# Kernel optimization log

Measured on AMD Instinct MI355X. Metric: run time of the kernel, lower is better.

## Reference

```python
import jax, jax.numpy as jnp
import numpy as np

N_NODES = 100000
N_EDGES = 3200000
DIMS = [32, 256, 1024, 1024, 256, 6]


def setup_inputs() -> dict:
    key = jax.random.key(0)
    ks = jax.random.split(key, 2 + 2 * 5)
    inp = {
        "x": jax.random.normal(ks[0], (N_NODES, DIMS[0]), dtype=jnp.float32),
        "edge_index": jax.random.randint(ks[1], (2, N_EDGES), 0, N_NODES, dtype=jnp.int64),
    }
    for i in range(5):
        fan_in, fan_out = DIMS[i], DIMS[i + 1]
        scale = (2.0 / (fan_in + fan_out)) ** 0.5  # glorot-ish
        inp[f"W{i+1}"] = jax.random.normal(ks[2 + 2 * i], (fan_in, fan_out), dtype=jnp.float32) * scale
        inp[f"b{i+1}"] = jnp.zeros((fan_out,), dtype=jnp.float32)
    return inp


def _gcn_forward(x, edge_index, Ws, bs):
    N = x.shape[0]
    # add self loops (PyG GCNConv default)
    loop = jnp.arange(N, dtype=edge_index.dtype)
    src = jnp.concatenate([edge_index[0], loop])
    dst = jnp.concatenate([edge_index[1], loop])
    # symmetric normalization: deg computed on target index (gcn_norm)
    deg = jax.ops.segment_sum(jnp.ones_like(dst, dtype=x.dtype), dst, num_segments=N)
    dinv = jnp.where(deg > 0, jax.lax.rsqrt(deg), 0.0)
    norm = (dinv[src] * dinv[dst])[:, None]  # [E+N, 1]

    def conv(h, W, b):
        h = h @ W                                    # dense linear
        msg = h[src] * norm                          # gather + scale
        agg = jax.ops.segment_sum(msg, dst, num_segments=N)  # scatter-add
        return agg + b

    h = x
    for i in range(4):
        h = jax.nn.relu(conv(h, Ws[i], bs[i]))
    return conv(h, Ws[4], bs[4])


def reference(x, edge_index, W1, b1, W2, b2, W3, b3, W4, b4, W5, b5):
    return _gcn_forward(x, edge_index, (W1, W2, W3, W4, W5), (b1, b2, b3, b4, b5))
```

## Files before the change

kernel.cpp:

```cpp
#include <hip/hip_runtime.h>

typedef unsigned char u8;
typedef unsigned short u16;
typedef unsigned int u32;
typedef __bf16 bf16_t;
typedef bf16_t bf16x8 __attribute__((ext_vector_type(8)));
typedef float f32x4 __attribute__((ext_vector_type(4)));
typedef float f32x2 __attribute__((ext_vector_type(2)));

#define LDS_PTR(p) ((__attribute__((address_space(3))) unsigned int*)(p))
#define GLB_PTR(p) ((const __attribute__((address_space(1))) unsigned int*)(p))

#define BSH 9
#define BCAP 32768

static __device__ __forceinline__ float bf2f(u16 h) {
  u32 u = ((u32)h) << 16;
  return __builtin_bit_cast(float, u);
}
static __device__ __forceinline__ u16 f2bf(float f) {
  u32 u = __builtin_bit_cast(u32, f);
  u += 0x7fffu + ((u >> 16) & 1u);
  return (u16)(u >> 16);
}

static __device__ __forceinline__ int xcd_swizzle(int wg, int nwg) {
  const int q = nwg >> 3, r = nwg & 7;
  const int xcd = wg & 7, pos = wg >> 3;
  return (xcd < r ? xcd * (q + 1) : r * (q + 1) + (xcd - r) * q) + pos;
}

__global__ void detect_kernel(const int* __restrict__ ei, const u16* __restrict__ x,
                              int* __restrict__ flags, int* __restrict__ zp, int zn) {
  __shared__ int cnt;
  if (threadIdx.x == 0) cnt = 0;
  __syncthreads();
  if (blockIdx.x == 0) {
    if (ei[1 + 2 * threadIdx.x] != 0) atomicAdd(&cnt, 1);
    __syncthreads();
    if (threadIdx.x == 0) flags[0] = (cnt == 0) ? 1 : 0;
  } else if (blockIdx.x == 1) {
    u32 u = x[threadIdx.x];
    u32 e = (u >> 7) & 0xFF;
    if (e >= 0x60 && e <= 0x83) atomicAdd(&cnt, 1);
    __syncthreads();
    if (threadIdx.x == 0) flags[1] = (cnt >= 240) ? 0 : 1;
  } else {
    for (int i = threadIdx.x; i < zn; i += 256) zp[i] = 0;
  }
}

static __device__ __forceinline__ int eidx(const void* ei, size_t i, int m) {
  return m ? (int)((const long long*)ei)[i] : ((const int*)ei)[i];
}

__global__ void zero_out_kernel(void* __restrict__ out, int n, const int* __restrict__ flags) {
  int i = blockIdx.x * 256 + threadIdx.x;
  if (i < n) {
    if (flags[1]) ((float*)out)[i] = 0.0f;
    else ((u16*)out)[i] = 0;
  }
}

struct CvtArgs {
  const void* src[10];
  u16* dst[10];
  int K[10];
  int N[10];
  int start[11];
};
__global__ void convert_all_kernel(CvtArgs a, const int* __restrict__ flags) {
  int idx = blockIdx.x * 256 + threadIdx.x;
  int f32 = flags[1];
#pragma unroll
  for (int t = 0; t < 10; ++t) {
    if (idx >= a.start[t] && idx < a.start[t + 1]) {
      int local = idx - a.start[t];
      int K = a.K[t], N = a.N[t];
      int k = local / N, n = local - k * N;
      float v = f32 ? ((const float*)a.src[t])[local] : bf2f(((const u16*)a.src[t])[local]);
      a.dst[t][(size_t)n * K + k] = f2bf(v);
    }
  }
}

__global__ __launch_bounds__(256) void bin_kernel(const void* __restrict__ ei,
                                                  int* __restrict__ gcur,
                                                  int2* __restrict__ pairs, int E, int Nn,
                                                  const int* __restrict__ flags, int nblk) {
  __shared__ int h[256];
  __shared__ int base[256];
  const int m = flags[0];
  const int nb = (Nn + (1 << BSH) - 1) >> BSH;
  const int per = (E + nblk - 1) / nblk;
  const int e0 = blockIdx.x * per;
  const int e1 = (e0 + per < E) ? e0 + per : E;
  for (int i = threadIdx.x; i < nb; i += 256) h[i] = 0;
  __syncthreads();
  for (int e = e0 + threadIdx.x; e < e1; e += 256) {
    int d = eidx(ei, (size_t)E + e, m);
    if ((u32)d < (u32)Nn) atomicAdd(&h[d >> BSH], 1);
  }
  __syncthreads();
  for (int i = threadIdx.x; i < nb; i += 256) {
    base[i] = atomicAdd(&gcur[i], h[i]);
    h[i] = 0;
  }
  __syncthreads();
  for (int e = e0 + threadIdx.x; e < e1; e += 256) {
    int d = eidx(ei, (size_t)E + e, m);
    if ((u32)d >= (u32)Nn) continue;
    int s = eidx(ei, (size_t)e, m);
    if ((u32)s >= (u32)Nn) s = 0;
    int b = d >> BSH;
    int p = base[b] + atomicAdd(&h[b], 1);
    if (p < BCAP) pairs[(size_t)b * BCAP + p] = make_int2(s, d);
  }
}

__global__ __launch_bounds__(256) void bucket_scan_kernel(const int* __restrict__ gcur,
                                                          int* __restrict__ gbase, int NB) {
  __shared__ int sd[256];
  int tid = threadIdx.x;
  int v = (tid < NB) ? gcur[tid] : 0;
  if (v > BCAP) v = BCAP;
  sd[tid] = v;
  __syncthreads();
  for (int s = 1; s < 256; s <<= 1) {
    int t = (tid >= s) ? sd[tid - s] : 0;
    __syncthreads();
    sd[tid] += t;
    __syncthreads();
  }
  if (tid < NB) gbase[tid] = sd[tid] - v;
}

__global__ __launch_bounds__(512) void bucket_finalize_kernel(
    const int2* __restrict__ pairs, const int* __restrict__ gcur,
    const int* __restrict__ gbase, int* __restrict__ rowp, float* __restrict__ dinv,
    int* __restrict__ csr, int Nn) {
  __shared__ int cnt[512];
  __shared__ int scn[512];
  const int b = blockIdx.x;
  const int n0 = b << BSH;
  const int tid = threadIdx.x;
  cnt[tid] = 0;
  __syncthreads();
  int tot = gcur[b];
  if (tot > BCAP) tot = BCAP;
  for (int i = tid; i < tot; i += 512) {
    int2 pr = pairs[(size_t)b * BCAP + i];
    atomicAdd(&cnt[pr.y - n0], 1);
  }
  __syncthreads();
  int myc = cnt[tid];
  scn[tid] = myc;
  __syncthreads();
  for (int s = 1; s < 512; s <<= 1) {
    int t = (tid >= s) ? scn[tid - s] : 0;
    __syncthreads();
    scn[tid] += t;
    __syncthreads();
  }
  const int node = n0 + tid;
  const int start = gbase[b] + scn[tid] - myc;
  if (node < Nn) {
    rowp[node] = start;
    dinv[node] = rsqrtf((float)(myc + 1));
    if (node == Nn - 1) rowp[Nn] = gbase[b] + scn[tid];
  }
  cnt[tid] = start;
  __syncthreads();
  for (int i = tid; i < tot; i += 512) {
    int2 pr = pairs[(size_t)b * BCAP + i];
    int p = atomicAdd(&cnt[pr.y - n0], 1);
    csr[p] = pr.x;
  }
}

template <int NPW, int ACT, bool SRCF, bool DSTF, bool EDGEW>
__global__ __launch_bounds__(256) void spmm_narrow_kernel(
    const void* __restrict__ Hb, void* __restrict__ Gb,
    const int* __restrict__ rowp, const int* __restrict__ csr,
    const float* __restrict__ dinv, const u16* __restrict__ bias,
    int relu, int Nn, int src_stride, int dst_stride, const int* __restrict__ flags) {
  constexpr int G = 64 / NPW;
  constexpr int B = 16;
  const int lane = threadIdx.x & 63;
  const int col = lane & (G - 1);
  const int node = blockIdx.x * 4 * NPW + (threadIdx.x >> 6) * NPW + (lane / G);
  const bool anode = node < Nn;
  const bool act = anode && (col < ACT);
  int sf32 = 0, of32 = 0;
  if (SRCF) sf32 = flags[1];
  if (DSTF) of32 = flags[1];
  const u16* Hs = (const u16*)Hb;
  const float* Hf = (const float*)Hb;

  int e0 = 0, cnt = 0;
  if (anode) {
    e0 = rowp[node];
    cnt = rowp[node + 1] - e0;
  }
  float acc = 0.0f;
  for (int jb = 0; jb < cnt; jb += B) {
    int s[B];
#pragma unroll
    for (int j = 0; j < B; ++j) {
      bool val = (jb + j) < cnt;
      s[j] = val ? csr[e0 + jb + j] : node;
    }
    float wv[B];
    if constexpr (EDGEW) {
#pragma unroll
      for (int j = 0; j < B; ++j) wv[j] = ((jb + j) < cnt) ? dinv[s[j]] : 0.0f;
    }
    float v[B];
#pragma unroll
    for (int j = 0; j < B; ++j) {
      bool val = act && ((jb + j) < cnt);
      size_t idx = (size_t)s[j] * src_stride + col;
      v[j] = val ? ((SRCF && sf32) ? Hf[idx] : bf2f(Hs[idx])) : 0.0f;
    }
#pragma unroll
    for (int j = 0; j < B; ++j) {
      if constexpr (EDGEW) acc += wv[j] * v[j];
      else acc += v[j];
    }
  }
  if (!act) return;
  const float wi = dinv[node];
  {
    size_t idx = (size_t)node * src_stride + col;
    float sv = (SRCF && sf32) ? Hf[idx] : bf2f(Hs[idx]);
    if constexpr (EDGEW) acc += wi * sv;
    else acc += sv;
  }
  float v = acc * wi;
  if (bias) v += bf2f(bias[col]);
  if (relu) v = fmaxf(v, 0.0f);
  size_t didx = (size_t)node * dst_stride + col;
  if (DSTF && of32) ((float*)Gb)[didx] = v;
  else ((u16*)Gb)[didx] = f2bf(v);
}

template <int W>
__global__ __launch_bounds__(256) void spmm_fp8_kernel(
    const u8* __restrict__ Hq, u16* __restrict__ Gout,
    const int* __restrict__ rowp, const int* __restrict__ csr,
    const float* __restrict__ dinv, int n0, int n1, int dst_stride) {
  constexpr int BPL = W / 64;
  constexpr int ND = BPL / 4;
  constexpr int B = (W == 1024) ? 8 : 16;
  const int lane = threadIdx.x & 63;
  const int node = __builtin_amdgcn_readfirstlane(n0 + blockIdx.x * 4 + (threadIdx.x >> 6));
  if (node >= n1) return;
  const int off = lane * BPL;
  f32x2 acc[2 * ND] = {};

  auto dec1 = [&](const u32* d) {
#pragma unroll
    for (int q = 0; q < ND; ++q) {
      f32x2 a = __builtin_amdgcn_cvt_pk_f32_fp8((int)d[q], false);
      f32x2 b = __builtin_amdgcn_cvt_pk_f32_fp8((int)d[q], true);
      acc[2 * q] += a;
      acc[2 * q + 1] += b;
    }
  };
  auto ldrow = [&](u32* v, int s) {
    const u8* p = Hq + (size_t)s * W + off;
    if constexpr (ND == 4) *(int4*)v = *(const int4*)p;
    else v[0] = *(const u32*)p;
  };

  const int e0 = rowp[node];
  const int cnt = rowp[node + 1] - e0;
  const int tot = cnt + 1;
  const int NB2 = (tot + B - 1) / B;
  const int NBF = NB2 - 1;

  u32 vA[B][ND], vB[B][ND];

  auto ldb_full = [&](u32 (*v)[ND], int k) {
    const int base = k * B;
    int s[B];
#pragma unroll
    for (int j = 0; j < B; ++j) s[j] = csr[e0 + base + j];
#pragma unroll
    for (int j = 0; j < B; ++j) ldrow(v[j], s[j]);
  };
  auto ldb_last = [&](u32 (*v)[ND]) {
    const int base = NBF * B;
#pragma unroll
    for (int j = 0; j < B; ++j) {
      const int i = base + j;
      if (i < tot) {
        int s = (i < cnt) ? csr[e0 + i] : node;
        ldrow(v[j], s);
      } else {
#pragma unroll
        for (int q = 0; q < ND; ++q) v[j][q] = 0u;
      }
    }
  };
  auto decfull = [&](u32 (*v)[ND]) {
#pragma unroll
    for (int j = 0; j < B; ++j) dec1(v[j]);
  };

  if (NB2 == 1) {
    ldb_last(vA);
    decfull(vA);
  } else {
    ldb_last(vA);
    ldb_full(vB, 0);
    int k = 1;
    while (k + 1 < NBF) {
      decfull(vA);
      ldb_full(vA, k);
      decfull(vB);
      ldb_full(vB, k + 1);
      k += 2;
    }
    if (k < NBF) {
      decfull(vA);
      ldb_full(vA, k);
      decfull(vB);
      decfull(vA);
    } else {
      decfull(vA);
      decfull(vB);
    }
  }

  const float wi = dinv[node];
  u32 d[2 * ND];
#pragma unroll
  for (int kk = 0; kk < 2 * ND; ++kk) {
    float v0 = acc[kk].x * wi, v1 = acc[kk].y * wi;
    d[kk] = (u32)f2bf(v0) | ((u32)f2bf(v1) << 16);
  }
  u16* gp = Gout + (size_t)(node - n0) * dst_stride + off;
  if constexpr (ND == 4) {
    ((int4*)gp)[0] = make_int4((int)d[0], (int)d[1], (int)d[2], (int)d[3]);
    ((int4*)gp)[1] = make_int4((int)d[4], (int)d[5], (int)d[6], (int)d[7]);
  } else {
    *(int2*)gp = make_int2((int)d[0], (int)d[1]);
  }
}

__global__ __launch_bounds__(256) void spmm_u8_kernel(
    const u8* __restrict__ Hq, u16* __restrict__ G,
    const int* __restrict__ rowp, const int* __restrict__ csr,
    const float* __restrict__ dinv, const u32* __restrict__ maxbits,
    const u16* __restrict__ bias, int relu, int Nn, int dst_stride) {
  constexpr int B = 16;
  const int lane = threadIdx.x & 63;
  const int node = __builtin_amdgcn_readfirstlane(blockIdx.x * 4 + (threadIdx.x >> 6));
  if (node >= Nn) return;
  const int off = lane * 4;
  float mx = __builtin_bit_cast(float, *maxbits);
  float sq = mx > 0.0f ? mx * (1.0f / 127.0f) : 0.0f;
  float a0 = 0.0f, a1 = 0.0f, a2 = 0.0f, a3 = 0.0f, wsum = 0.0f;

  auto dec1 = [&](u32 d, float w) {
    a0 += w * (float)(d & 0xffu);
    a1 += w * (float)((d >> 8) & 0xffu);
    a2 += w * (float)((d >> 16) & 0xffu);
    a3 += w * (float)(d >> 24);
    wsum += w;
  };
  auto ldrow = [&](u32* v, int s) { *v = *(const u32*)(Hq + (size_t)s * 256 + off); };

  const int e0 = rowp[node];
  const int cnt = rowp[node + 1] - e0;
  const int tot = cnt + 1;
  const int NB2 = (tot + B - 1) / B;
  const int NBF = NB2 - 1;

  u32 vA[B], vB[B];
  float wA[B], wB[B];

  auto ldb_full = [&](u32* v, float* wv, int k) {
    const int base = k * B;
    int s[B];
#pragma unroll
    for (int j = 0; j < B; ++j) s[j] = csr[e0 + base + j];
#pragma unroll
    for (int j = 0; j < B; ++j) wv[j] = dinv[s[j]];
#pragma unroll
    for (int j = 0; j < B; ++j) ldrow(&v[j], s[j]);
  };
  auto ldb_last = [&](u32* v, float* wv) {
    const int base = NBF * B;
#pragma unroll
    for (int j = 0; j < B; ++j) {
      const int i = base + j;
      if (i < tot) {
        int s = (i < cnt) ? csr[e0 + i] : node;
        wv[j] = dinv[s];
        ldrow(&v[j], s);
      } else {
        v[j] = 0u;
        wv[j] = 0.0f;
      }
    }
  };
  auto decfull = [&](u32* v, float* wv) {
#pragma unroll
    for (int j = 0; j < B; ++j) dec1(v[j], wv[j]);
  };

  if (NB2 == 1) {
    ldb_last(vA, wA);
    decfull(vA, wA);
  } else {
    ldb_last(vA, wA);
    ldb_full(vB, wB, 0);
    int k = 1;
    while (k + 1 < NBF) {
      decfull(vA, wA);
      ldb_full(vA, wA, k);
      decfull(vB, wB);
      ldb_full(vB, wB, k + 1);
      k += 2;
    }
    if (k < NBF) {
      decfull(vA, wA);
      ldb_full(vA, wA, k);
      decfull(vB, wB);
      decfull(vA, wA);
    } else {
      decfull(vA, wA);
      decfull(vB, wB);
    }
  }

  const float wi = dinv[node];
  float su[4] = {a0, a1, a2, a3};
  float vals[4];
#pragma unroll
  for (int k2 = 0; k2 < 4; ++k2) {
    float v = (su[k2] - 128.0f * wsum) * wi * sq;
    if (bias) v += bf2f(bias[off + k2]);
    if (relu) v = fmaxf(v, 0.0f);
    vals[k2] = v;
  }
  u32 d0 = (u32)f2bf(vals[0]) | ((u32)f2bf(vals[1]) << 16);
  u32 d1 = (u32)f2bf(vals[2]) | ((u32)f2bf(vals[3]) << 16);
  *(int2*)(G + (size_t)node * dst_stride + off) = make_int2((int)d0, (int)d1);
}

__global__ void quant_kernel(const u16* __restrict__ t4, u8* __restrict__ t4q,
                             const u32* __restrict__ maxbits, int n4) {
  int i = blockIdx.x * 256 + threadIdx.x;
  if (i >= n4) return;
  float mx = __builtin_bit_cast(float, *maxbits);
  float inv = mx > 0.0f ? 127.0f / mx : 0.0f;
  int2 v = ((const int2*)t4)[i];
  float f0 = bf2f((u16)(v.x & 0xffff)), f1 = bf2f((u16)((u32)v.x >> 16));
  float f2 = bf2f((u16)(v.y & 0xffff)), f3 = bf2f((u16)((u32)v.y >> 16));
  int q0 = (int)rintf(f0 * inv), q1 = (int)rintf(f1 * inv);
  int q2 = (int)rintf(f2 * inv), q3 = (int)rintf(f3 * inv);
  q0 = min(127, max(-127, q0)) + 128; q1 = min(127, max(-127, q1)) + 128;
  q2 = min(127, max(-127, q2)) + 128; q3 = min(127, max(-127, q3)) + 128;
  ((u32*)t4q)[i] = (u32)q0 | ((u32)q1 << 8) | ((u32)q2 << 16) | ((u32)q3 << 24);
}

__global__ __launch_bounds__(256) void gemm_fast_kernel(
    const u16* __restrict__ A, int lda, const u16* __restrict__ Bt,
    u16* __restrict__ C, int ldc, const u16* __restrict__ bias,
    int M, int N, int K, int relu, int fp8out, u32* __restrict__ maxout,
    const float* __restrict__ rowscale) {
  __shared__ __align__(16) u16 sA[128 * 64];
  __shared__ __align__(16) u16 sB[128 * 64];
  const int tid = threadIdx.x;
  const int lane = tid & 63;
  const int wave = __builtin_amdgcn_readfirstlane(tid >> 6);
  const int gx = gridDim.x;
  int wg = blockIdx.y * gx + blockIdx.x;
  wg = xcd_swizzle(wg, gx * gridDim.y);
  const int m0 = (wg / gx) * 128, n0 = (wg % gx) * 128;
  const int wm = (wave & 1) * 64, wn = (wave >> 1) * 64;
  const int lr = lane & 15, lq = lane >> 4;
  const int lrow = lane >> 3;
  const int lcol = (lane & 7) * 8;
  f32x4 acc[4][4] = {};

  for (int kb = 0; kb < K; kb += 64) {
#pragma unroll
    for (int it = 0; it < 4; ++it) {
      const int rbase = (it * 4 + wave) * 8;
      int gm = m0 + rbase + lrow;
      if (gm >= M) gm = M - 1;
      __builtin_amdgcn_global_load_lds(GLB_PTR(A + (size_t)gm * lda + kb + lcol),
                                       LDS_PTR(sA + rbase * 64), 16, 0, 0);
      const int gn = n0 + rbase + lrow;
      __builtin_amdgcn_global_load_lds(GLB_PTR(Bt + (size_t)gn * K + kb + lcol),
                                       LDS_PTR(sB + rbase * 64), 16, 0, 0);
    }
    __syncthreads();
#pragma unroll
    for (int ks = 0; ks < 2; ++ks) {
      bf16x8 af[4], bfr[4];
#pragma unroll
      for (int i = 0; i < 4; ++i)
        af[i] = *(const bf16x8*)(sA + (wm + i * 16 + lr) * 64 + ks * 32 + lq * 8);
#pragma unroll
      for (int i = 0; i < 4; ++i)
        bfr[i] = *(const bf16x8*)(sB + (wn + i * 16 + lr) * 64 + ks * 32 + lq * 8);
#pragma unroll
      for (int im = 0; im < 4; ++im)
#pragma unroll
        for (int in = 0; in < 4; ++in)
          acc[im][in] = __builtin_amdgcn_mfma_f32_16x16x32_bf16(af[im], bfr[in], acc[im][in], 0, 0, 0);
    }
    __syncthreads();
  }
  u32 mymax = 0;
#pragma unroll
  for (int im = 0; im < 4; ++im) {
    f32x4 rs4;
    if (rowscale) {
      rs4 = *(const f32x4*)(rowscale + (m0 + wm + im * 16 + lq * 4));
    }
#pragma unroll
    for (int in = 0; in < 4; ++in) {
      int col = n0 + wn + in * 16 + lr;
      float bv = bias ? bf2f(bias[col]) : 0.0f;
#pragma unroll
      for (int r = 0; r < 4; ++r) {
        int row = m0 + wm + im * 16 + lq * 4 + r;
        if (row < M) {
          float v = acc[im][in][r] + bv;
          if (relu) v = fmaxf(v, 0.0f);
          if (rowscale) v *= rs4[r];
          if (maxout) {
            u32 ab = __builtin_bit_cast(u32, v) & 0x7fffffffu;
            mymax = mymax > ab ? mymax : ab;
          }
          if (fp8out) {
            int pk = __builtin_amdgcn_cvt_pk_fp8_f32(v, v, 0, false);
            ((u8*)C)[(size_t)row * ldc + col] = (u8)(pk & 0xff);
          } else {
            C[(size_t)row * ldc + col] = f2bf(v);
          }
        }
      }
    }
  }
  if (maxout) {
    u32* red = (u32*)sA;
    red[tid] = mymax;
    __syncthreads();
    for (int s = 128; s > 0; s >>= 1) {
      if (tid < s) red[tid] = red[tid] > red[tid + s] ? red[tid] : red[tid + s];
      __syncthreads();
    }
    if (tid == 0) atomicMax(maxout, red[0]);
  }
}

#define LP 72
__global__ __launch_bounds__(256) void gemm_small_kernel(
    const u16* __restrict__ A, int lda, const u16* __restrict__ Bt,
    u16* __restrict__ C, int ldc, const u16* __restrict__ bias,
    int M, int N, int K, int relu, int fp8out, const float* __restrict__ rowscale) {
  __shared__ __align__(16) u16 sA[128 * LP];
  __shared__ __align__(16) u16 sB[128 * LP];
  const int tid = threadIdx.x;
  const int lane = tid & 63, wave = tid >> 6;
  const int gx = gridDim.x;
  int wg = blockIdx.y * gx + blockIdx.x;
  wg = xcd_swizzle(wg, gx * gridDim.y);
  const int m0 = (wg / gx) * 128, n0 = (wg % gx) * 128;
  const int wm = (wave & 1) * 64, wn = (wave >> 1) * 64;
  const int lr = lane & 15;
  const int lq = lane >> 4;
  f32x4 acc[4][4] = {};

  for (int kb = 0; kb < K; kb += 64) {
#pragma unroll
    for (int it = 0; it < 4; ++it) {
      int linear = it * 2048 + tid * 8;
      int row = linear >> 6, kc = linear & 63;
      int gm = m0 + row, gk = kb + kc;
      int4 v = make_int4(0, 0, 0, 0);
      if (gm < M && gk < K) v = *(const int4*)(A + (size_t)gm * lda + gk);
      *(int4*)(sA + row * LP + kc) = v;
    }
#pragma unroll
    for (int it = 0; it < 4; ++it) {
      int linear = it * 2048 + tid * 8;
      int row = linear >> 6, kc = linear & 63;
      int gn = n0 + row, gk = kb + kc;
      int4 v = make_int4(0, 0, 0, 0);
      if (gn < N && gk < K) v = *(const int4*)(Bt + (size_t)gn * K + gk);
      *(int4*)(sB + row * LP + kc) = v;
    }
    __syncthreads();
#pragma unroll
    for (int ks = 0; ks < 2; ++ks) {
      bf16x8 af[4], bfr[4];
#pragma unroll
      for (int i = 0; i < 4; ++i)
        af[i] = *(const bf16x8*)(sA + (wm + i * 16 + lr) * LP + ks * 32 + lq * 8);
#pragma unroll
      for (int i = 0; i < 4; ++i)
        bfr[i] = *(const bf16x8*)(sB + (wn + i * 16 + lr) * LP + ks * 32 + lq * 8);
#pragma unroll
      for (int im = 0; im < 4; ++im)
#pragma unroll
        for (int in = 0; in < 4; ++in)
          acc[im][in] = __builtin_amdgcn_mfma_f32_16x16x32_bf16(af[im], bfr[in], acc[im][in], 0, 0, 0);
    }
    __syncthreads();
  }
#pragma unroll
  for (int im = 0; im < 4; ++im) {
    f32x4 rs4;
    if (rowscale) rs4 = *(const f32x4*)(rowscale + (m0 + wm + im * 16 + lq * 4));
#pragma unroll
    for (int in = 0; in < 4; ++in) {
      int col = n0 + wn + in * 16 + lr;
      if (col >= N) continue;
      float bv = bias ? bf2f(bias[col]) : 0.0f;
#pragma unroll
      for (int r = 0; r < 4; ++r) {
        int row = m0 + wm + im * 16 + lq * 4 + r;
        if (row < M) {
          float v = acc[im][in][r] + bv;
          if (relu) v = fmaxf(v, 0.0f);
          if (rowscale) v *= rs4[r];
          if (fp8out) {
            int pk = __builtin_amdgcn_cvt_pk_fp8_f32(v, v, 0, false);
            ((u8*)C)[(size_t)row * ldc + col] = (u8)(pk & 0xff);
          } else {
            C[(size_t)row * ldc + col] = f2bf(v);
          }
        }
      }
    }
  }
}

extern "C" void kernel_launch(void* const* d_in, const int* in_sizes, int n_in,
                              void* d_out, int out_size, void* d_ws, size_t ws_size,
                              hipStream_t stream) {
  const u16* x  = (const u16*)d_in[0];
  const int* ei = (const int*)d_in[1];

  const int Nn = in_sizes[0] / 32;
  const int E  = in_sizes[1] / 2;
  const int NB = (Nn + (1 << BSH) - 1) >> BSH;

  char* w = (char*)d_ws;
  size_t off = 0;
  auto alloc = [&](size_t bytes) -> void* {
    void* p = w + off;
    off = (off + bytes + 255) & ~(size_t)255;
    return p;
  };
  int*   flags  = (int*)alloc(256);
  int*   gcur   = (int*)alloc(1024);
  int*   gbase  = (int*)alloc(1024);
  u32*   tmax   = (u32*)alloc(256);
  int*   rowp   = (int*)alloc((size_t)(Nn + 1) * 4);
  float* dinv   = (float*)alloc((size_t)Nn * 4);
  int*   csr    = (int*)alloc((size_t)E * 4);
  u16*   Wt1    = (u16*)alloc((size_t)32 * 256 * 2);
  u16*   Wt2    = (u16*)alloc((size_t)256 * 1024 * 2);
  u16*   Wt3    = (u16*)alloc((size_t)1024 * 1024 * 2);
  u16*   Wt4    = (u16*)alloc((size_t)1024 * 256 * 2);
  u16*   Wt5    = (u16*)alloc((size_t)256 * 6 * 2);
  u16*   bc1    = (u16*)alloc(256 * 2);
  u16*   bc2    = (u16*)alloc(1024 * 2);
  u16*   bc3    = (u16*)alloc(1024 * 2);
  u16*   bc4    = (u16*)alloc(256 * 2);
  u16*   bc5    = (u16*)alloc(6 * 2);

  const size_t fixed_end = off;
  const size_t hbytes = (size_t)Nn * 1024 * 2;
  auto align256 = [](size_t b) { return (b + 255) & ~(size_t)255; };
  int CH = Nn / 4;
  if (CH < 1) CH = 1;
  {
    size_t need = fixed_end + align256((size_t)CH * 1024 * 2) + align256(hbytes);
    if (ws_size < need) CH = (Nn + 7) / 8;
  }
  while ((size_t)CH * 1024 < (size_t)Nn * 32) CH *= 2;
  const int NR = (Nn + CH - 1) / CH;

  u16*   S      = (u16*)alloc((size_t)CH * 1024 * 2);
  u16*   H      = (u16*)alloc(hbytes);
  const size_t required = off;
  (void)n_in;

  if (ws_size < required) {
    if (ws_size >= 4096) {
      detect_kernel<<<3, 256, 0, stream>>>(ei, x, flags, gcur, 576);
      zero_out_kernel<<<(out_size + 255) / 256, 256, 0, stream>>>(d_out, out_size, flags);
    }
    return;
  }

  u8*  h2q = (u8*)H;
  u8*  t4q = (u8*)H;
  u16* g2  = H + (size_t)Nn * 512;
  u16* t4  = H + (size_t)Nn * 512;
  u8*  h1q = (u8*)(H + (size_t)Nn * 768);
  u16* h3R = H + (size_t)Nn * 768;
  u16* h4  = H + (size_t)Nn * 768;

  int2* pairs = (int2*)H;

  detect_kernel<<<3, 256, 0, stream>>>(ei, x, flags, gcur, 576);
  bin_kernel<<<1024, 256, 0, stream>>>(ei, gcur, pairs, E, Nn, flags, 1024);
  bucket_scan_kernel<<<1, 256, 0, stream>>>(gcur, gbase, NB);
  bucket_finalize_kernel<<<NB, 512, 0, stream>>>(pairs, gcur, gbase, rowp, dinv, csr, Nn);

  {
    CvtArgs a;
    const int Ks[10] = {32, 1, 256, 1, 1024, 1, 1024, 1, 256, 1};
    const int Ns[10] = {256, 256, 1024, 1024, 1024, 1024, 256, 256, 6, 6};
    u16* ds[10] = {Wt1, bc1, Wt2, bc2, Wt3, bc3, Wt4, bc4, Wt5, bc5};
    int cum = 0;
    for (int t = 0; t < 10; ++t) {
      a.src[t] = d_in[2 + t];
      a.dst[t] = ds[t];
      a.K[t] = Ks[t];
      a.N[t] = Ns[t];
      a.start[t] = cum;
      cum += Ks[t] * Ns[t];
    }
    a.start[10] = cum;
    convert_all_kernel<<<(cum + 255) / 256, 256, 0, stream>>>(a, flags);
  }

  const int sg = (Nn + 3) / 4;
  const int mb = (Nn + 127) / 128;

  spmm_narrow_kernel<2, 32, true, false, true><<<(Nn + 7) / 8, 256, 0, stream>>>(
      x, S, rowp, csr, dinv, nullptr, 0, Nn, 32, 32, flags);
  gemm_small_kernel<<<dim3(2, mb), 256, 0, stream>>>(S, 32, Wt1, (u16*)h1q, 256, bc1,
                                                     Nn, 256, 32, 1, 1, dinv);

  spmm_fp8_kernel<256><<<sg, 256, 0, stream>>>(h1q, g2, rowp, csr, dinv, 0, Nn, 256);
  gemm_fast_kernel<<<dim3(8, mb), 256, 0, stream>>>(g2, 256, Wt2, (u16*)h2q, 1024, bc2,
                                                    Nn, 1024, 256, 1, 1, nullptr, dinv);

  for (int R = 0; R < NR; ++R) {
    int n0 = R * CH;
    int n1 = n0 + CH < Nn ? n0 + CH : Nn;
    int MR = n1 - n0;
    int mbr = (MR + 127) / 128;
    spmm_fp8_kernel<1024><<<(MR + 3) / 4, 256, 0, stream>>>(h2q, S, rowp, csr, dinv, n0, n1, 1024);
    gemm_fast_kernel<<<dim3(8, mbr), 256, 0, stream>>>(S, 1024, Wt3, h3R, 1024, bc3,
                                                       MR, 1024, 1024, 1, 0, nullptr, nullptr);
    gemm_fast_kernel<<<dim3(2, mbr), 256, 0, stream>>>(h3R, 1024, Wt4, t4 + (size_t)n0 * 256, 256,
                                                       nullptr, MR, 256, 1024, 0, 0, tmax, nullptr);
  }

  quant_kernel<<<(Nn * 64 + 255) / 256, 256, 0, stream>>>(t4, t4q, tmax, Nn * 64);

  spmm_u8_kernel<<<sg, 256, 0, stream>>>(t4q, h4, rowp, csr, dinv, tmax, bc4, 1, Nn, 256);

  gemm_small_kernel<<<dim3(1, mb), 256, 0, stream>>>(h4, 256, Wt5, S, 6, nullptr,
                                                     Nn, 6, 256, 0, 0, nullptr);
  spmm_narrow_kernel<8, 6, false, true, true><<<(Nn + 31) / 32, 256, 0, stream>>>(
      S, d_out, rowp, csr, dinv, bc5, 0, Nn, 6, 6, flags);
}
```

Baseline: 2.099 ms.

## Add 256x256-tile GEMM kernel with 512 threads for layer-3 linear

Adds a new GEMM kernel using 256x256 output tiles, 8 waves, and double-buffered 128KB LDS staging via global_load_lds with XOR swizzle. It replaces the 128x128-tile kernel for the 1024x1024 layer-3 matmul. Larger tiles raise arithmetic intensity and cut global/L2 traffic per FLOP. The trade-offs are lower occupancy, higher register pressure from 32 accumulators per lane, and per-element scalar stores in the epilogue. A runtime launch-error check falls back to the old kernel.

New measurement: 1.889 ms. -10.0%, faster.

```diff
diff --git a/kernel.cpp b/kernel.cpp
--- a/kernel.cpp
+++ b/kernel.cpp
@@ -465,6 +465,117 @@
   q0 = min(127, max(-127, q0)) + 128; q1 = min(127, max(-127, q1)) + 128;
   q2 = min(127, max(-127, q2)) + 128; q3 = min(127, max(-127, q3)) + 128;
   ((u32*)t4q)[i] = (u32)q0 | ((u32)q1 << 8) | ((u32)q2 << 16) | ((u32)q3 << 24);
+}
+
+__global__ __launch_bounds__(512) void gemm256_kernel(
+    const u16* __restrict__ A, int lda, const u16* __restrict__ Bt, int ldb,
+    u16* __restrict__ C, int ldc, const u16* __restrict__ bias,
+    int M, int K, int relu) {
+  extern __shared__ u16 lds[];
+  u16* ldsA = lds;
+  u16* ldsB = lds + 32768;
+  const int tid = threadIdx.x;
+  const int lane = tid & 63;
+  const int wid = __builtin_amdgcn_readfirstlane(tid >> 6);
+  const int wr = wid >> 2, wc = wid & 3;
+  const int lr = lane & 15, lq = lane >> 4;
+  const int gx = gridDim.x;
+  int wg = blockIdx.y * gx + blockIdx.x;
+  wg = xcd_swizzle(wg, gx * gridDim.y);
+  const int m0 = (wg / gx) * 256, n0 = (wg % gx) * 256;
+
+  f32x4 acc[8][4] = {};
+
+  auto STAGE = [&](int b, int kb) {
+#pragma unroll
+    for (int it = 0; it < 4; ++it) {
+      int slot = it * 512 + tid;
+      int row = slot >> 3, blk = slot & 7;
+      int gm = m0 + row;
+      if (gm >= M) gm = M - 1;
+      int gcol = kb * 64 + ((blk ^ (row & 7)) << 3);
+      __builtin_amdgcn_global_load_lds(GLB_PTR(A + (size_t)gm * lda + gcol),
+                                       LDS_PTR(ldsA + (size_t)b * 16384 + slot * 8), 16, 0, 0);
+    }
+#pragma unroll
+    for (int it = 0; it < 4; ++it) {
+      int slot = it * 512 + tid;
+      int row = slot >> 3, blk = slot & 7;
+      int gn = n0 + row;
+      int gcol = kb * 64 + ((blk ^ (row & 7)) << 3);
+      __builtin_amdgcn_global_load_lds(GLB_PTR(Bt + (size_t)gn * ldb + gcol),
+                                       LDS_PTR(ldsB + (size_t)b * 16384 + slot * 8), 16, 0, 0);
+    }
+  };
+
+  auto COMPUTE = [&](int b) {
+    const u16* Ab = ldsA + (size_t)b * 16384;
+    const u16* Bb = ldsB + (size_t)b * 16384;
+#pragma unroll
+    for (int ks = 0; ks < 2; ++ks) {
+      bf16x8 af[8], bfr[4];
+#pragma unroll
+      for (int i = 0; i < 8; ++i) {
+        int R = wr * 128 + i * 16 + lr;
+        af[i] = *(const bf16x8*)(Ab + R * 64 + ((ks * 32 + lq * 8) ^ ((R & 7) << 3)));
+      }
+#pragma unroll
+      for (int j = 0; j < 4; ++j) {
+        int S = wc * 64 + j * 16 + lr;
+        bfr[j] = *(const bf16x8*)(Bb + S * 64 + ((ks * 32 + lq * 8) ^ ((S & 7) << 3)));
+      }
+#pragma unroll
+      for (int i = 0; i < 8; ++i)
+#pragma unroll
+        for (int j = 0; j < 4; ++j)
+          acc[i][j] = __builtin_amdgcn_mfma_f32_16x16x32_bf16(af[i], bfr[j], acc[i][j], 0, 0, 0);
+    }
+  };
+
+  const int nk = K >> 6;
+  STAGE(0, 0);
+  STAGE(1, 1);
+  asm volatile("s_waitcnt vmcnt(8)" ::: "memory");
+  __builtin_amdgcn_sched_barrier(0);
+  __builtin_amdgcn_s_barrier();
+  __builtin_amdgcn_sched_barrier(0);
+
+  for (int k = 0; k < nk; ++k) {
+    const int cur = k & 1;
+    COMPUTE(cur);
+    if (k + 1 < nk) {
+      __builtin_amdgcn_sched_barrier(0);
+      __builtin_amdgcn_s_barrier();
+      __builtin_amdgcn_sched_barrier(0);
+      if (k + 2 < nk) {
+        STAGE(cur, k + 2);
+        asm volatile("s_waitcnt vmcnt(8)" ::: "memory");
+      } else {
+        asm volatile("s_waitcnt vmcnt(0)" ::: "memory");
+      }
+      __builtin_amdgcn_sched_barrier(0);
+      __builtin_amdgcn_s_barrier();
+      __builtin_amdgcn_sched_barrier(0);
+    }
+  }
+
+#pragma unroll
+  for (int i = 0; i < 8; ++i) {
+#pragma unroll
+    for (int j = 0; j < 4; ++j) {
+      int col = n0 + wc * 64 + j * 16 + lr;
+      float bv = bias ? bf2f(bias[col]) : 0.0f;
+#pragma unroll
+      for (int r = 0; r < 4; ++r) {
+        int row = m0 + wr * 128 + i * 16 + lq * 4 + r;
+        if (row < M) {
+          float v = acc[i][j][r] + bv;
+          if (relu) v = fmaxf(v, 0.0f);
+          C[(size_t)row * ldc + col] = f2bf(v);
+        }
+      }
+    }
+  }
 }
 
 __global__ __launch_bounds__(256) void gemm_fast_kernel(
@@ -749,14 +860,26 @@
   gemm_fast_kernel<<<dim3(8, mb), 256, 0, stream>>>(g2, 256, Wt2, (u16*)h2q, 1024, bc2,
                                                     Nn, 1024, 256, 1, 1, nullptr, dinv);
 
+  (void)hipGetLastError();
+  bool use256 = true;
   for (int R = 0; R < NR; ++R) {
     int n0 = R * CH;
     int n1 = n0 + CH < Nn ? n0 + CH : Nn;
     int MR = n1 - n0;
     int mbr = (MR + 127) / 128;
     spmm_fp8_kernel<1024><<<(MR + 3) / 4, 256, 0, stream>>>(h2q, S, rowp, csr, dinv, n0, n1, 1024);
-    gemm_fast_kernel<<<dim3(8, mbr), 256, 0, stream>>>(S, 1024, Wt3, h3R, 1024, bc3,
-                                                       MR, 1024, 1024, 1, 0, nullptr, nullptr);
+    if (use256) {
+      int mtr = (MR + 255) / 256;
+      gemm256_kernel<<<dim3(4, mtr), 512, 131072, stream>>>(S, 1024, Wt3, 1024, h3R, 1024,
+                                                            bc3, MR, 1024, 1);
+      if (hipGetLastError() != hipSuccess) {
+        use256 = false;
+      }
+    }
+    if (!use256) {
+      gemm_fast_kernel<<<dim3(8, mbr), 256, 0, stream>>>(S, 1024, Wt3, h3R, 1024, bc3,
+                                                         MR, 1024, 1024, 1, 0, nullptr, nullptr);
+    }
     gemm_fast_kernel<<<dim3(2, mbr), 256, 0, stream>>>(h3R, 1024, Wt4, t4 + (size_t)n0 * 256, 256,
                                                        nullptr, MR, 256, 1024, 0, 0, tmax, nullptr);
   }
```
